# Performance work log

Measured on AMD Instinct MI355X. Metric: run time of the kernel, lower is better.

The kernel has to match this reference:

```python
import jax, jax.numpy as jnp
import numpy as np

B = 16384       # batch rows
N_IN = 8192     # input bits per row (columns of x)
N_GATES = 8192  # gates in this row


def setup_inputs() -> dict:
    key = jax.random.key(0)
    k_x, k_g, k_c = jax.random.split(key, 3)
    # binary activations entering the gate row
    x = jax.random.randint(k_x, (B, N_IN), 0, 2).astype(jnp.bool_)
    # per-gate 4-entry truth table (the discretized gate function)
    gates = jax.random.randint(k_g, (N_GATES, 4), 0, 2).astype(jnp.bool_)
    # per-gate pair of input wire indices into the N_IN columns of x
    choices = jax.random.randint(k_c, (N_GATES, 2), 0, N_IN, dtype=jnp.int32)
    return {"x": x, "gates": gates, "choices": choices}


def reference(x, gates, choices):
    n_gates = gates.shape[0]
    # gather the two chosen input bits per gate: [B, n_gates, 2]
    chosen = x[:, choices.reshape(-1)].reshape(x.shape[0], n_gates, 2)
    # 2-bit lookup index into the truth table: a*2 + b in {0,1,2,3}
    idx = chosen[:, :, 0].astype(jnp.int32) * 2 + chosen[:, :, 1].astype(jnp.int32)
    # out[b, g] = gates[g, idx[b, g]]  (advanced indexing broadcasts (1,G) x (B,G))
    out = gates[jnp.arange(n_gates)[None, :], idx]
    return out
```

## Files before the change

### kernel.cpp

```cpp
#include <hip/hip_runtime.h>
#include <stdint.h>


static constexpr int BATCH  = 16384;
static constexpr int N_IN   = 8192;
static constexpr int NG     = 8192;
static constexpr int ROWS   = 8;
static constexpr int BLK    = 256;
static constexpr int GPT    = 4;
static constexpr int NGROUP = NG / (BLK * GPT);

typedef uint32_t u32x4 __attribute__((ext_vector_type(4)));
typedef int      i32x2 __attribute__((ext_vector_type(2)));

__device__ __forceinline__ bool wave_detect_i32(u32x4 w) {
    return __ballot((((w.x | w.y | w.z | w.w) & ~1u) == 0u)) == ~0ULL;
}

__global__ __launch_bounds__(BLK) void pack_meta(
        const int* __restrict__ choices,
        const void* __restrict__ gates_,
        uint32_t* __restrict__ meta) {
    const int g = blockIdx.x * BLK + threadIdx.x;
    const bool i32 = wave_detect_i32(((const u32x4*)gates_)[g & 2047]);
    i32x2 c = ((const i32x2*)choices)[g];
    uint32_t tt;
    if (i32) {
        u32x4 gw = ((const u32x4*)gates_)[g];
        tt = (gw.x & 1u) | ((gw.y & 1u) << 1)
           | ((gw.z & 1u) << 2) | ((gw.w & 1u) << 3);
    } else {
        const uint8_t* gt = (const uint8_t*)gates_ + 4 * (long)g;
        tt = (uint32_t)gt[0] | ((uint32_t)gt[1] << 1)
           | ((uint32_t)gt[2] << 2) | ((uint32_t)gt[3] << 3);
    }
    meta[g] = (uint32_t)c.x | ((uint32_t)c.y << 13) | (tt << 26);
}

template <bool PACKED>
__global__ __launch_bounds__(BLK) void gate_main(
        const void*     __restrict__ xv,
        const uint32_t* __restrict__ meta,
        const int*      __restrict__ choices,
        const void*     __restrict__ gates_,
        uint32_t*       __restrict__ out) {
    __shared__ uint8_t xp[N_IN];
    const int  t  = threadIdx.x;
    const long b0 = (long)blockIdx.x * ROWS;

    const bool i32 = wave_detect_i32(
        ((const u32x4*)xv)[blockIdx.x * BLK + t]);

    if (i32) {
        const uint32_t* x = (const uint32_t*)xv;
        uint32_t* dst = (uint32_t*)xp;
        #pragma unroll
        for (int i = 0; i < N_IN / 4 / BLK; ++i) {
            const int o = t + i * BLK;
            uint32_t pb = 0;
            #pragma unroll
            for (int r = 0; r < ROWS; ++r) {
                const u32x4* src = (const u32x4*)(x + (b0 + r) * (long)N_IN) + o;
                u32x4 v = __builtin_nontemporal_load(src);
                pb |= (v.x << r) | (v.y << (r + 8))
                    | (v.z << (r + 16)) | (v.w << (r + 24));
            }
            dst[o] = pb;
        }
    } else {
        const u32x4* xr  = (const u32x4*)((const uint8_t*)xv + b0 * N_IN);
        u32x4*       dst = (u32x4*)xp;
        #pragma unroll
        for (int i = 0; i < N_IN / 16 / BLK; ++i) {
            const int o = t + i * BLK;
            u32x4 p = (u32x4){0u, 0u, 0u, 0u};
            #pragma unroll
            for (int r = 0; r < ROWS; ++r) {
                u32x4 v = __builtin_nontemporal_load(
                    &xr[(size_t)r * (N_IN / 16) + o]);
                p.x |= v.x << r;  p.y |= v.y << r;
                p.z |= v.z << r;  p.w |= v.w << r;
            }
            dst[o] = p;
        }
    }
    __syncthreads();

    u32x4 mq[NGROUP];
    if (PACKED) {
        #pragma unroll
        for (int k = 0; k < NGROUP; ++k)
            mq[k] = ((const u32x4*)meta)[k * BLK + t];
    } else {
        const bool gi32 = wave_detect_i32(
            ((const u32x4*)gates_)[(blockIdx.x * BLK + t) & 2047]);
        #pragma unroll
        for (int k = 0; k < NGROUP; ++k) {
            const int gb = k * BLK * GPT + t * GPT;
            #pragma unroll
            for (int j = 0; j < GPT; ++j) {
                const int g = gb + j;
                i32x2 c = ((const i32x2*)choices)[g];
                uint32_t tt;
                if (gi32) {
                    u32x4 gw = ((const u32x4*)gates_)[g];
                    tt = (gw.x & 1u) | ((gw.y & 1u) << 1)
                       | ((gw.z & 1u) << 2) | ((gw.w & 1u) << 3);
                } else {
                    const uint8_t* gt = (const uint8_t*)gates_ + 4 * (long)g;
                    tt = (uint32_t)gt[0] | ((uint32_t)gt[1] << 1)
                       | ((uint32_t)gt[2] << 2) | ((uint32_t)gt[3] << 3);
                }
                mq[k][j] = (uint32_t)c.x | ((uint32_t)c.y << 13) | (tt << 26);
            }
        }
    }

    #pragma unroll
    for (int k = 0; k < NGROUP; ++k) {
        const int gbase = k * BLK * GPT + t * GPT;

        uint32_t res[ROWS][GPT];
        #pragma unroll
        for (int j = 0; j < GPT; ++j) {
            const uint32_t mv = mq[k][j];
            const uint32_t v0 = xp[mv & 8191u];
            const uint32_t v1 = xp[(mv >> 13) & 8191u];
            const uint32_t tt = mv >> 26;
            #pragma unroll
            for (int r = 0; r < ROWS; ++r) {
                const uint32_t idx = (((v0 >> r) & 1u) << 1) | ((v1 >> r) & 1u);
                res[r][j] = (tt >> idx) & 1u;
            }
        }

        #pragma unroll
        for (int r = 0; r < ROWS; ++r) {
            u32x4 v = { res[r][0], res[r][1], res[r][2], res[r][3] };
            u32x4* dst = (u32x4*)(out + (b0 + r) * (long)NG + gbase);
            __builtin_nontemporal_store(v, dst);
        }
    }
}

extern "C" void kernel_launch(void* const* d_in, const int* in_sizes, int n_in,
                              void* d_out, int out_size, void* d_ws, size_t ws_size,
                              hipStream_t stream) {
    const void* x       = d_in[0];
    const void* gates   = d_in[1];
    const int*  choices = (const int*)d_in[2];
    uint32_t*   out     = (uint32_t*)d_out;

    if (ws_size >= NG * sizeof(uint32_t)) {
        uint32_t* meta = (uint32_t*)d_ws;
        pack_meta<<<NG / BLK, BLK, 0, stream>>>(choices, gates, meta);
        gate_main<true><<<BATCH / ROWS, BLK, 0, stream>>>(
            x, meta, choices, gates, out);
    } else {
        gate_main<false><<<BATCH / ROWS, BLK, 0, stream>>>(
            x, nullptr, choices, gates, out);
    }
}
```

Before: 829.7 us.

## Split row staging into two halves to overlap loads with compute and stores

Each block's 8 rows are now staged into shared memory in two halves of 4 rows, using a double buffer. The second half's global loads are issued before the first half is computed and stored, so load latency can overlap with work inside one block. The byte-gate truth-table packing also changes from four byte loads to a single word load and a multiply bit-gather. The cost is twice the shared memory per block, which may reduce occupancy, plus an extra barrier.

Result: no change. 817.3 us (-1.5%).

```diff
diff --git a/kernel.cpp b/kernel.cpp
--- a/kernel.cpp
+++ b/kernel.cpp
@@ -6,6 +6,7 @@
 static constexpr int N_IN   = 8192;
 static constexpr int NG     = 8192;
 static constexpr int ROWS   = 8;
+static constexpr int HALF   = 4;
 static constexpr int BLK    = 256;
 static constexpr int GPT    = 4;
 static constexpr int NGROUP = NG / (BLK * GPT);
@@ -30,9 +31,8 @@
         tt = (gw.x & 1u) | ((gw.y & 1u) << 1)
            | ((gw.z & 1u) << 2) | ((gw.w & 1u) << 3);
     } else {
-        const uint8_t* gt = (const uint8_t*)gates_ + 4 * (long)g;
-        tt = (uint32_t)gt[0] | ((uint32_t)gt[1] << 1)
-           | ((uint32_t)gt[2] << 2) | ((uint32_t)gt[3] << 3);
+        uint32_t gw = ((const uint32_t*)gates_)[g];
+        tt = ((gw & 0x01010101u) * 0x01020408u) >> 24;
     }
     meta[g] = (uint32_t)c.x | ((uint32_t)c.y << 13) | (tt << 26);
 }
@@ -44,47 +44,12 @@
         const int*      __restrict__ choices,
         const void*     __restrict__ gates_,
         uint32_t*       __restrict__ out) {
-    __shared__ uint8_t xp[N_IN];
+    __shared__ uint8_t xp[2][N_IN];
     const int  t  = threadIdx.x;
     const long b0 = (long)blockIdx.x * ROWS;
 
-    const bool i32 = wave_detect_i32(
+    const bool xi32 = wave_detect_i32(
         ((const u32x4*)xv)[blockIdx.x * BLK + t]);
-
-    if (i32) {
-        const uint32_t* x = (const uint32_t*)xv;
-        uint32_t* dst = (uint32_t*)xp;
-        #pragma unroll
-        for (int i = 0; i < N_IN / 4 / BLK; ++i) {
-            const int o = t + i * BLK;
-            uint32_t pb = 0;
-            #pragma unroll
-            for (int r = 0; r < ROWS; ++r) {
-                const u32x4* src = (const u32x4*)(x + (b0 + r) * (long)N_IN) + o;
-                u32x4 v = __builtin_nontemporal_load(src);
-                pb |= (v.x << r) | (v.y << (r + 8))
-                    | (v.z << (r + 16)) | (v.w << (r + 24));
-            }
-            dst[o] = pb;
-        }
-    } else {
-        const u32x4* xr  = (const u32x4*)((const uint8_t*)xv + b0 * N_IN);
-        u32x4*       dst = (u32x4*)xp;
-        #pragma unroll
-        for (int i = 0; i < N_IN / 16 / BLK; ++i) {
-            const int o = t + i * BLK;
-            u32x4 p = (u32x4){0u, 0u, 0u, 0u};
-            #pragma unroll
-            for (int r = 0; r < ROWS; ++r) {
-                u32x4 v = __builtin_nontemporal_load(
-                    &xr[(size_t)r * (N_IN / 16) + o]);
-                p.x |= v.x << r;  p.y |= v.y << r;
-                p.z |= v.z << r;  p.w |= v.w << r;
-            }
-            dst[o] = p;
-        }
-    }
-    __syncthreads();
 
     u32x4 mq[NGROUP];
     if (PACKED) {
@@ -92,14 +57,12 @@
         for (int k = 0; k < NGROUP; ++k)
             mq[k] = ((const u32x4*)meta)[k * BLK + t];
     } else {
-        const bool gi32 = wave_detect_i32(
-            ((const u32x4*)gates_)[(blockIdx.x * BLK + t) & 2047]);
+        const bool gi32 = wave_detect_i32(((const u32x4*)gates_)[t]);
         #pragma unroll
         for (int k = 0; k < NGROUP; ++k) {
-            const int gb = k * BLK * GPT + t * GPT;
             #pragma unroll
             for (int j = 0; j < GPT; ++j) {
-                const int g = gb + j;
+                const int g = k * BLK * GPT + t * GPT + j;
                 i32x2 c = ((const i32x2*)choices)[g];
                 uint32_t tt;
                 if (gi32) {
@@ -107,40 +70,87 @@
                     tt = (gw.x & 1u) | ((gw.y & 1u) << 1)
                        | ((gw.z & 1u) << 2) | ((gw.w & 1u) << 3);
                 } else {
-                    const uint8_t* gt = (const uint8_t*)gates_ + 4 * (long)g;
-                    tt = (uint32_t)gt[0] | ((uint32_t)gt[1] << 1)
-                       | ((uint32_t)gt[2] << 2) | ((uint32_t)gt[3] << 3);
+                    uint32_t gw = ((const uint32_t*)gates_)[g];
+                    tt = ((gw & 0x01010101u) * 0x01020408u) >> 24;
                 }
                 mq[k][j] = (uint32_t)c.x | ((uint32_t)c.y << 13) | (tt << 26);
             }
         }
     }
 
-    #pragma unroll
-    for (int k = 0; k < NGROUP; ++k) {
-        const int gbase = k * BLK * GPT + t * GPT;
-
-        uint32_t res[ROWS][GPT];
-        #pragma unroll
-        for (int j = 0; j < GPT; ++j) {
-            const uint32_t mv = mq[k][j];
-            const uint32_t v0 = xp[mv & 8191u];
-            const uint32_t v1 = xp[(mv >> 13) & 8191u];
-            const uint32_t tt = mv >> 26;
+    auto stage = [&](int h) {
+        const long rb = b0 + h * HALF;
+        if (xi32) {
+            const uint32_t* x = (const uint32_t*)xv;
+            uint32_t* dst = (uint32_t*)xp[h];
             #pragma unroll
-            for (int r = 0; r < ROWS; ++r) {
-                const uint32_t idx = (((v0 >> r) & 1u) << 1) | ((v1 >> r) & 1u);
-                res[r][j] = (tt >> idx) & 1u;
+            for (int i = 0; i < N_IN / 4 / BLK; ++i) {
+                const int o = t + i * BLK;
+                uint32_t pb = 0;
+                #pragma unroll
+                for (int r = 0; r < HALF; ++r) {
+                    const u32x4* src =
+                        (const u32x4*)(x + (rb + r) * (long)N_IN) + o;
+                    u32x4 v = __builtin_nontemporal_load(src);
+                    pb |= (v.x << r) | (v.y << (r + 8))
+                        | (v.z << (r + 16)) | (v.w << (r + 24));
+                }
+                dst[o] = pb;
+            }
+        } else {
+            const u32x4* xr =
+                (const u32x4*)((const uint8_t*)xv + rb * N_IN);
+            u32x4* dst = (u32x4*)xp[h];
+            #pragma unroll
+            for (int i = 0; i < N_IN / 16 / BLK; ++i) {
+                const int o = t + i * BLK;
+                u32x4 p = (u32x4){0u, 0u, 0u, 0u};
+                #pragma unroll
+                for (int r = 0; r < HALF; ++r) {
+                    u32x4 v = __builtin_nontemporal_load(
+                        &xr[(size_t)r * (N_IN / 16) + o]);
+                    p.x |= v.x << r;  p.y |= v.y << r;
+                    p.z |= v.z << r;  p.w |= v.w << r;
+                }
+                dst[o] = p;
             }
         }
+    };
 
+    auto compute_store = [&](int h) {
+        const long rb = b0 + h * HALF;
         #pragma unroll
-        for (int r = 0; r < ROWS; ++r) {
-            u32x4 v = { res[r][0], res[r][1], res[r][2], res[r][3] };
-            u32x4* dst = (u32x4*)(out + (b0 + r) * (long)NG + gbase);
-            __builtin_nontemporal_store(v, dst);
+        for (int k = 0; k < NGROUP; ++k) {
+            const int gbase = k * BLK * GPT + t * GPT;
+            uint32_t res[HALF][GPT];
+            #pragma unroll
+            for (int j = 0; j < GPT; ++j) {
+                const uint32_t mv = mq[k][j];
+                const uint32_t v0 = xp[h][mv & 8191u];
+                const uint32_t v1 = xp[h][(mv >> 13) & 8191u];
+                const uint32_t tt = mv >> 26;
+                #pragma unroll
+                for (int r = 0; r < HALF; ++r) {
+                    const uint32_t idx =
+                        (((v0 >> r) & 1u) << 1) | ((v1 >> r) & 1u);
+                    res[r][j] = (tt >> idx) & 1u;
+                }
+            }
+            #pragma unroll
+            for (int r = 0; r < HALF; ++r) {
+                u32x4 v = { res[r][0], res[r][1], res[r][2], res[r][3] };
+                u32x4* dst = (u32x4*)(out + (rb + r) * (long)NG + gbase);
+                __builtin_nontemporal_store(v, dst);
+            }
         }
-    }
+    };
+
+    stage(0);
+    __syncthreads();
+    stage(1);
+    compute_store(0);
+    __syncthreads();
+    compute_store(1);
 }
 
 extern "C" void kernel_launch(void* const* d_in, const int* in_sizes, int n_in,
```
